# Performance work log

Measured on AMD Instinct MI355X. Metric: run time of the kernel, lower is better.

## Reference

```python
import jax, jax.numpy as jnp
import numpy as np
from jax import lax

N, T, E = 20000, 64, 640000
H, OUT, HEADS = 128, 64, 3
NEG_SLOPE = 0.2  # GATConv default negative_slope


def setup_inputs() -> dict:
    key = jax.random.key(0)
    ks = jax.random.split(key, 10)
    s = 0.1
    return {
        "node_features": jax.random.normal(ks[0], (N, T), jnp.float32),
        "edge_index": jax.random.randint(ks[1], (2, E), 0, N, dtype=jnp.int32),
        "edge_attributes": jax.random.uniform(ks[2], (E,), jnp.float32),
        "lstm_Wih": jax.random.normal(ks[3], (4 * H, 1), jnp.float32) * s,
        "lstm_Whh": jax.random.normal(ks[4], (4 * H, H), jnp.float32) * s,
        "lstm_bih": jnp.zeros((4 * H,), jnp.float32),
        "lstm_bhh": jnp.zeros((4 * H,), jnp.float32),
        "gcn_W": jax.random.normal(ks[5], (H, H), jnp.float32) * s,
        "gcn_b": jnp.zeros((H,), jnp.float32),
        "gat_W": jax.random.normal(ks[6], (HEADS * OUT, H), jnp.float32) * s,
        "gat_att_src": jax.random.normal(ks[7], (HEADS, OUT), jnp.float32) * s,
        "gat_att_dst": jax.random.normal(ks[8], (HEADS, OUT), jnp.float32) * s,
        "gat_b": jnp.zeros((HEADS * OUT,), jnp.float32),
    }


def _lstm_last(x, Wih, Whh, bih, bhh):
    """x: [N, T, 1] -> last hidden state [N, H] (torch gate order i,f,g,o)."""
    n = x.shape[0]
    h_dim = Whh.shape[1]
    b = bih + bhh

    def step(carry, xt):
        h, c = carry
        g = xt @ Wih.T + h @ Whh.T + b  # [N, 4H]
        i, f, gg, o = jnp.split(g, 4, axis=-1)
        c = jax.nn.sigmoid(f) * c + jax.nn.sigmoid(i) * jnp.tanh(gg)
        h = jax.nn.sigmoid(o) * jnp.tanh(c)
        return (h, c), None

    init = (jnp.zeros((n, h_dim), x.dtype), jnp.zeros((n, h_dim), x.dtype))
    (h, _), _ = lax.scan(step, init, jnp.swapaxes(x, 0, 1))
    return h


def _add_self_loops(row, col, n):
    loop = jnp.arange(n, dtype=row.dtype)
    return jnp.concatenate([row, loop]), jnp.concatenate([col, loop])


def _gcn(x, row, col, edge_weight, W, b):
    """PyG GCNConv: self-loops (weight 1), symmetric normalization, W x + b."""
    n = x.shape[0]
    row, col = _add_self_loops(row, col, n)
    ew = jnp.concatenate([edge_weight, jnp.ones((n,), edge_weight.dtype)])
    x = x @ W.T  # [N, H]
    deg = jax.ops.segment_sum(ew, col, num_segments=n)
    dinv = jnp.where(deg > 0, deg ** -0.5, 0.0)
    norm = dinv[row] * ew * dinv[col]  # [E+N]
    out = jax.ops.segment_sum(x[row] * norm[:, None], col, num_segments=n)
    return out + b


def _gat(x, row, col, W, att_src, att_dst, b):
    """PyG GATConv (concat=True): self-loops, edge softmax over incoming edges."""
    n = x.shape[0]
    heads, c = att_src.shape
    xh = (x @ W.T).reshape(n, heads, c)  # [N, Hd, C]
    a_src = jnp.einsum('nhc,hc->nh', xh, att_src)  # [N, Hd]
    a_dst = jnp.einsum('nhc,hc->nh', xh, att_dst)
    row, col = _add_self_loops(row, col, n)
    alpha = jax.nn.leaky_relu(a_src[row] + a_dst[col], NEG_SLOPE)  # [E', Hd]
    amax = jax.ops.segment_max(alpha, col, num_segments=n)
    alpha = jnp.exp(alpha - amax[col])
    denom = jax.ops.segment_sum(alpha, col, num_segments=n)
    alpha = alpha / denom[col]
    out = jax.ops.segment_sum(xh[row] * alpha[:, :, None], col, num_segments=n)
    return out.reshape(n, heads * c) + b


def reference(node_features, edge_index, edge_attributes,
              lstm_Wih, lstm_Whh, lstm_bih, lstm_bhh,
              gcn_W, gcn_b, gat_W, gat_att_src, gat_att_dst, gat_b):
    x = node_features[:, :, None]  # [N, T, 1]
    x = _lstm_last(x, lstm_Wih, lstm_Whh, lstm_bih, lstm_bhh)  # [N, H]
    x = jax.nn.relu(x)
    row, col = edge_index[0], edge_index[1]
    x = _gcn(x, row, col, edge_attributes, gcn_W, gcn_b)
    x = jax.nn.relu(x)
    x = _gat(x, row, col, gat_W, gat_att_src, gat_att_dst, gat_b)  # [N, Hd*C]
    return jnp.mean(x, axis=0, keepdims=True)  # global_mean_pool, batch=None -> [1, Hd*C]
```

## Files before the change

kernel.cpp:

```cpp
#include <hip/hip_runtime.h>


#define N_NODES 20000
#define T_STEPS 64
#define N_EDGES 640000
#define HDIM    128
#define JOUT    192
#define NEG_SLOPE 0.2f
#define EDGE_CAP 128
#define NBW     16
#define NGRP    6
#define NBB     (NBW * NGRP)
#define BTHR    768
#define NBLK    209
#define GRIDX   215
#define LDS_W     131072
#define LDS_BW    4096
#define LDS_SCR   (NGRP * 4096)
#define LDS_FLG   256
#define LDS_TOTAL (LDS_W + LDS_BW + LDS_SCR + LDS_FLG)

#define L2E  1.4426950408889634f
#define K2E  2.8853900817779268f

typedef _Float16 half8 __attribute__((ext_vector_type(8)));
typedef _Float16 half4v __attribute__((ext_vector_type(4)));
typedef _Float16 half2v __attribute__((ext_vector_type(2)));
typedef float floatx4 __attribute__((ext_vector_type(4)));

__device__ __forceinline__ float lrelu(float x) { return x > 0.f ? x : NEG_SLOPE * x; }

__global__ __launch_bounds__(256) void prep_kernel(
    const float* __restrict__ Whh, _Float16* __restrict__ Wpack,
    const float* __restrict__ gcnW, _Float16* __restrict__ WpackG,
    const float* __restrict__ gatW, _Float16* __restrict__ WpackA,
    int* __restrict__ cnt, float* __restrict__ deg,
    float* __restrict__ Wgt, float* __restrict__ accum)
{
  const int b = blockIdx.x;
  const int tid = threadIdx.x;
  if (b < 32) {
    int i = b * 256 + tid;
    int tile = i >> 6, lane = i & 63;
    int nt = tile >> 2, kt = tile & 3;
    int row = nt * 16 + (lane & 15);
    int c0  = kt * 32 + (lane >> 4) * 8;
    const float sc = ((row >> 7) == 2) ? K2E : L2E;
    half8 v;
    #pragma unroll
    for (int j = 0; j < 8; ++j)
      v[j] = (_Float16)(Whh[row * 128 + c0 + j] * sc);
    *(half8*)&Wpack[(size_t)i * 8] = v;
  } else if (b < 40) {
    int i = (b - 32) * 256 + tid;
    int tile = i >> 6, lane = i & 63;
    int mt = tile >> 2, kt = tile & 3;
    int row = mt * 16 + (lane & 15);
    int c0  = kt * 32 + (lane >> 4) * 8;
    half8 v;
    #pragma unroll
    for (int j = 0; j < 8; ++j) v[j] = (_Float16)gcnW[row * 128 + c0 + j];
    *(half8*)&WpackG[(size_t)i * 8] = v;
  } else if (b < 52) {
    int i = (b - 40) * 256 + tid;
    int tile = i >> 6, lane = i & 63;
    int mt = tile >> 2, kt = tile & 3;
    int row = mt * 16 + (lane & 15);
    int c0  = kt * 32 + (lane >> 4) * 8;
    half8 v;
    #pragma unroll
    for (int j = 0; j < 8; ++j) v[j] = (_Float16)gatW[row * 128 + c0 + j];
    *(half8*)&WpackA[(size_t)i * 8] = v;
  } else {
    int i = (b - 52) * 256 + tid;
    if (i < N_NODES) {
      cnt[i] = 0;
      deg[i] = 0.f;
      *(float4*)&Wgt[i * 4] = make_float4(0.f, 0.f, 0.f, 0.f);
    }
    if (i < JOUT) accum[i] = 0.f;
  }
}


#define INITACC(L, acc) do {                                                  \
  _Pragma("unroll") for (int g_ = 0; g_ < 4; ++g_) {                          \
    const float4 p0_ = *(const float4*)&bwRole[g_ * 128 + (L) * 16];          \
    const float4 p1_ = *(const float4*)&bwRole[g_ * 128 + (L) * 16 + 2];      \
    acc[g_][0] = p0_.x + xv * p0_.y;                                          \
    acc[g_][1] = p0_.z + xv * p0_.w;                                          \
    acc[g_][2] = p1_.x + xv * p1_.y;                                          \
    acc[g_][3] = p1_.z + xv * p1_.w;                                          \
  }                                                                           \
} while (0)

#define LDA(buf, L, KT) do {                                                  \
  _Pragma("unroll") for (int g_ = 0; g_ < 4; ++g_)                            \
    buf[g_] = *(const half8*)&WlRole[g_ * 16384 + (L) * 2048 + (KT) * 512];   \
} while (0)

#define MFA(acc, buf, KT) do {                                                \
  _Pragma("unroll") for (int g_ = 0; g_ < 4; ++g_)                            \
    acc[g_] = __builtin_amdgcn_mfma_f32_16x16x32_f16(                         \
        buf[g_], Bf[(KT)], acc[g_], 0, 0, 0);                                 \
} while (0)

#define PHASE4(L, acc) do {                                                   \
  const int cg_ = cgb + (L);                                                  \
  half4v hpack;                                                               \
  _Pragma("unroll") for (int r_ = 0; r_ < 4; ++r_) {                          \
    const float Be = __builtin_amdgcn_exp2f(-acc[0][r_]);                     \
    const float Ae = __builtin_amdgcn_exp2f(-acc[1][r_]);                     \
    const float De = __builtin_amdgcn_exp2f(acc[2][r_]);                      \
    const float Ee = __builtin_amdgcn_exp2f(-acc[3][r_]);                     \
    const float Ap = Ae + 1.f;                                                \
    const float Bp = Be + 1.f;                                                \
    const float Dp = De + 1.f;                                                \
    const float Nn = cst[(L) * 4 + r_] * Bp * Dp + Ap * (De - 1.f);           \
    const float cv = Nn * __builtin_amdgcn_rcpf(Ap * Bp * Dp);                \
    cst[(L) * 4 + r_] = cv;                                                   \
    const float cvc = fminf(fmaxf(cv, -10.f), 10.f);                          \
    const float Fe = __builtin_amdgcn_exp2f(K2E * cvc);                       \
    hpack[r_] = (_Float16)((Fe - 1.f) *                                       \
                __builtin_amdgcn_rcpf((Ee + 1.f) * (Fe + 1.f)));              \
  }                                                                           \
  const int lp_ = nl + 16 * (2 * (cg_ & 1) + wq_hi);                          \
  *(half4v*)&myscr[(cg_ >> 1) * 512 + lp_ * 8 + j0] = hpack;                  \
} while (0)

#define SB __builtin_amdgcn_sched_barrier(0)

#define SIGNAL(arr, val) do {                                                 \
  __threadfence_block();                                                      \
  if (ln == 0) arr[wv] = (val);                                               \
} while (0)
#define WAITGE(arr, val) do {                                                 \
  if (ln == 0) { while (arr[pw] < (val)) __builtin_amdgcn_s_sleep(1); }       \
  __builtin_amdgcn_wave_barrier();                                            \
  __threadfence_block();                                                      \
} while (0)

#define LSTM_STEP(t) do {                                                     \
  WAITGE(flW, (t));                                                           \
  half8 Bf[4];                                                                \
  _Pragma("unroll") for (int kt_ = 0; kt_ < 4; ++kt_)                         \
    Bf[kt_] = *(const half8*)&scrLane[kt_ * 512];                             \
  SIGNAL(flR, (t) + 1);                                                       \
  floatx4 accA[4], accB[4];                                                   \
  half8 Aa[4], Ab[4];                                                         \
                                                                  \
  INITACC(0, accA);                                                           \
  LDA(Aa, 0, 0); LDA(Ab, 0, 1);                                               \
  MFA(accA, Aa, 0); LDA(Aa, 0, 2);                                            \
  MFA(accA, Ab, 1); LDA(Ab, 0, 3);                                            \
  MFA(accA, Aa, 2); MFA(accA, Ab, 3);                                         \
                                                                  \
  INITACC(1, accB); LDA(Aa, 1, 0); LDA(Ab, 1, 1);                             \
  WAITGE(flR, (t) + 1);                                                       \
  SB; PHASE4(0, accA);                                                        \
  MFA(accB, Aa, 0); LDA(Aa, 1, 2);                                            \
  MFA(accB, Ab, 1); LDA(Ab, 1, 3);                                            \
  MFA(accB, Aa, 2); MFA(accB, Ab, 3);                                         \
                                                                  \
  INITACC(2, accA); LDA(Aa, 2, 0); LDA(Ab, 2, 1);                             \
  SB; PHASE4(1, accB);                                                        \
  MFA(accA, Aa, 0); LDA(Aa, 2, 2);                                            \
  MFA(accA, Ab, 1); LDA(Ab, 2, 3);                                            \
  MFA(accA, Aa, 2); MFA(accA, Ab, 3);                                         \
                                                                  \
  INITACC(3, accB); LDA(Aa, 3, 0); LDA(Ab, 3, 1);                             \
  SB; PHASE4(2, accA);                                                        \
  MFA(accB, Aa, 0); LDA(Aa, 3, 2);                                            \
  MFA(accB, Ab, 1); LDA(Ab, 3, 3);                                            \
  MFA(accB, Aa, 2); MFA(accB, Ab, 3);                                         \
  PHASE4(3, accB);                                                            \
  SIGNAL(flW, (t) + 1);                                                       \
} while (0)

__global__ __attribute__((amdgpu_flat_work_group_size(BTHR, BTHR),
                          amdgpu_waves_per_eu(3, 3)))
void lstm_stream_kernel(
    const float* __restrict__ xfeat, const _Float16* __restrict__ Wpack,
    const float* __restrict__ Wih, const float* __restrict__ bih,
    const float* __restrict__ bhh, _Float16* __restrict__ x1,
    const int* __restrict__ ei, const float* __restrict__ ew,
    int* __restrict__ cnt, int2* __restrict__ pairB, float* __restrict__ deg)
{
  extern __shared__ char dynlds[];
  const int tid  = threadIdx.x;

  if (blockIdx.x >= NBLK) {
    float* ldeg = (float*)dynlds;
    for (int i = tid; i < N_NODES; i += BTHR) ldeg[i] = 0.f;
    __syncthreads();
    const int stride = (GRIDX - NBLK) * BTHR;
    for (int e = (blockIdx.x - NBLK) * BTHR + tid; e < N_EDGES; e += stride) {
      const int r = ei[e];
      const int c = ei[N_EDGES + e];
      const float w = ew[e];
      const int p = atomicAdd(&cnt[c], 1);
      pairB[(size_t)c * EDGE_CAP + p] = make_int2(r, __float_as_int(w));
      atomicAdd(&ldeg[c], w);
    }
    __syncthreads();
    for (int i = tid; i < N_NODES; i += BTHR) {
      const float v = ldeg[i];
      if (v != 0.f) atomicAdd(&deg[i], v);
    }
    return;
  }

  _Float16* Wl  = (_Float16*)dynlds;
  float2*   bw  = (float2*)(dynlds + LDS_W);
  _Float16* scr = (_Float16*)(dynlds + LDS_W + LDS_BW);
  volatile int* flR = (volatile int*)(dynlds + LDS_W + LDS_BW + LDS_SCR);
  volatile int* flW = flR + 16;

  const int wv   = tid >> 6;
  const int pw   = wv ^ 1;
  const int grp  = wv >> 1;
  const int role = wv & 1;
  const int cgb  = role * 4;
  const int ln   = tid & 63;
  const int nl   = ln & 15;
  const int quad = ln >> 4;
  const int n0   = blockIdx.x * NBB + grp * NBW;
  const int node  = n0 + nl;
  const int nodeC = (node < N_NODES) ? node : (N_NODES - 1);

  {
    const float4* src = (const float4*)Wpack;
    float4* dst = (float4*)Wl;
    for (int i = tid; i < LDS_W / 16; i += BTHR) dst[i] = src[i];
  }
  for (int i = tid; i < 512; i += BTHR) {
    const float sc = ((i >> 7) == 2) ? K2E : L2E;
    bw[i] = make_float2((bih[i] + bhh[i]) * sc, Wih[i] * sc);
  }
  {
    float4* z = (float4*)scr;
    for (int i = tid; i < LDS_SCR / 16; i += BTHR)
      z[i] = make_float4(0.f, 0.f, 0.f, 0.f);
  }
  if (tid < 32) { flR[tid] = 0; }
  __syncthreads();

  _Float16* myscr = scr + grp * 2048;
  const _Float16* WlRole  = Wl + (size_t)cgb * 2048 + (size_t)ln * 8;
  const float2*   bwRole  = bw + cgb * 16 + quad * 4;
  const _Float16* scrLane = myscr + (size_t)ln * 8;
  const float* xrow = xfeat + (size_t)nodeC * T_STEPS;

  float cst[16];
  #pragma unroll
  for (int i = 0; i < 16; ++i) cst[i] = 0.f;

  const int wq_hi = quad >> 1;
  const int j0    = (quad & 1) * 4;

  float xv = xrow[0];

  #pragma unroll 1
  for (int t = 0; t < T_STEPS; ++t) {
    const float xn = xrow[(t + 1 <= 63) ? (t + 1) : 63];
    LSTM_STEP(t);
    xv = xn;
  }

  if (node < N_NODES) {
    #pragma unroll
    for (int k = 0; k < 2; ++k) {
      const int kt = role * 2 + k;
      half8 hf = *(const half8*)&scrLane[kt * 512];
      #pragma unroll
      for (int j = 0; j < 8; ++j)
        hf[j] = (_Float16)fmaxf((float)hf[j], 0.f);
      *(half8*)&x1[(size_t)node * HDIM + kt * 32 + quad * 8] = hf;
    }
  }
}

__global__ __launch_bounds__(256) void agg_gemm_att_kernel(
    const _Float16* __restrict__ x1, const float* __restrict__ deg,
    const int* __restrict__ cnt, const int2* __restrict__ pairB,
    const float* __restrict__ gcn_b,
    const _Float16* __restrict__ PG, const _Float16* __restrict__ PA,
    const float* __restrict__ att_src, const float* __restrict__ att_dst,
    _Float16* __restrict__ xh, float4* __restrict__ asrc,
    float4* __restrict__ adst)
{
  __shared__ float2 stg[4][64];
  __shared__ _Float16 z[16][132];
  __shared__ _Float16 zz[16][132];
  __shared__ float aS[JOUT], aD[JOUT];
  __shared__ float sAp[4][16][3], sDp[4][16][3];

  const int tid = threadIdx.x;
  const int ln = tid & 63;
  const int wv = tid >> 6;
  const int quad = ln >> 4;
  const int nl = ln & 15;
  const int nb = blockIdx.x * 16;

  for (int i = tid; i < JOUT; i += 256) { aS[i] = att_src[i]; aD[i] = att_dst[i]; }

  const half2v* x12 = (const half2v*)x1;
  #pragma unroll 1
  for (int d = 0; d < 4; ++d) {
    const int c = nb + wv * 4 + d;
    const float dc = rsqrtf(deg[c] + 1.0f);
    const half2v xc = x12[c * 64 + ln];
    float ax = (float)xc[0] * dc * dc, ay = (float)xc[1] * dc * dc;
    const int cc = cnt[c];
    const size_t base = (size_t)c * EDGE_CAP;
    for (int tb = 0; tb < cc; tb += 64) {
      const int ne = min(64, cc - tb);
      const int k = tb + ln;
      if (k < cc) {
        const int2 pr = pairB[base + k];
        stg[wv][ln] = make_float2(__int_as_float(pr.x),
            __int_as_float(pr.y) * rsqrtf(deg[pr.x] + 1.0f) * dc);
      }
      __builtin_amdgcn_wave_barrier();
      int i = 0;
      for (; i + 4 <= ne; i += 4) {
        float2 p0 = stg[wv][i],     p1 = stg[wv][i + 1];
        float2 p2 = stg[wv][i + 2], p3 = stg[wv][i + 3];
        const half2v a0 = x12[(size_t)__float_as_int(p0.x) * 64 + ln];
        const half2v a1 = x12[(size_t)__float_as_int(p1.x) * 64 + ln];
        const half2v a2 = x12[(size_t)__float_as_int(p2.x) * 64 + ln];
        const half2v a3 = x12[(size_t)__float_as_int(p3.x) * 64 + ln];
        ax += (float)a0[0] * p0.y + (float)a1[0] * p1.y +
              (float)a2[0] * p2.y + (float)a3[0] * p3.y;
        ay += (float)a0[1] * p0.y + (float)a1[1] * p1.y +
              (float)a2[1] * p2.y + (float)a3[1] * p3.y;
      }
      for (; i < ne; ++i) {
        float2 p0 = stg[wv][i];
        const half2v a0 = x12[(size_t)__float_as_int(p0.x) * 64 + ln];
        ax += (float)a0[0] * p0.y; ay += (float)a0[1] * p0.y;
      }
      __builtin_amdgcn_wave_barrier();
    }
    const int dn = wv * 4 + d;
    half2v o; o[0] = (_Float16)ax; o[1] = (_Float16)ay;
    *(half2v*)&z[dn][ln * 2] = o;
  }
  __syncthreads();

  {
    half8 Bf[4];
    #pragma unroll
    for (int kt = 0; kt < 4; ++kt)
      Bf[kt] = *(const half8*)&z[nl][kt * 32 + quad * 8];
    #pragma unroll
    for (int mm = 0; mm < 2; ++mm) {
      const int m = wv * 2 + mm;
      floatx4 acc = {0.f, 0.f, 0.f, 0.f};
      #pragma unroll
      for (int kt = 0; kt < 4; ++kt) {
        const half8 Af = *(const half8*)&PG[(size_t)((m * 4 + kt) * 64 + ln) * 8];
        acc = __builtin_amdgcn_mfma_f32_16x16x32_f16(Af, Bf[kt], acc, 0, 0, 0);
      }
      #pragma unroll
      for (int j = 0; j < 4; ++j) {
        const int jj = m * 16 + quad * 4 + j;
        zz[nl][jj] = (_Float16)fmaxf(acc[j] + gcn_b[jj], 0.f);
      }
    }
  }
  __syncthreads();

  {
    half8 Bf[4];
    #pragma unroll
    for (int kt = 0; kt < 4; ++kt)
      Bf[kt] = *(const half8*)&zz[nl][kt * 32 + quad * 8];
    float sA[3] = {0.f, 0.f, 0.f}, sD[3] = {0.f, 0.f, 0.f};
    #pragma unroll
    for (int mm = 0; mm < 3; ++mm) {
      const int m = wv * 3 + mm;
      floatx4 acc = {0.f, 0.f, 0.f, 0.f};
      #pragma unroll
      for (int kt = 0; kt < 4; ++kt) {
        const half8 Af = *(const half8*)&PA[(size_t)((m * 4 + kt) * 64 + ln) * 8];
        acc = __builtin_amdgcn_mfma_f32_16x16x32_f16(Af, Bf[kt], acc, 0, 0, 0);
      }
      const int h  = m >> 2;
      const int jo = (m & 3) * 16 + quad * 4;
      half4v o;
      #pragma unroll
      for (int j = 0; j < 4; ++j) {
        sA[h] += acc[j] * aS[h * 64 + jo + j];
        sD[h] += acc[j] * aD[h * 64 + jo + j];
        o[j] = (_Float16)acc[j];
      }
      *(half4v*)&xh[(size_t)(nb + nl) * JOUT + m * 16 + quad * 4] = o;
    }
    #pragma unroll
    for (int h = 0; h < 3; ++h) {
      sA[h] += __shfl_xor(sA[h], 16); sA[h] += __shfl_xor(sA[h], 32);
      sD[h] += __shfl_xor(sD[h], 16); sD[h] += __shfl_xor(sD[h], 32);
    }
    if (quad == 0) {
      #pragma unroll
      for (int h = 0; h < 3; ++h) {
        sAp[wv][nl][h] = sA[h];
        sDp[wv][nl][h] = sD[h];
      }
    }
  }
  __syncthreads();
  if (tid < 16) {
    float a0 = 0.f, a1 = 0.f, a2 = 0.f, d0 = 0.f, d1 = 0.f, d2 = 0.f;
    #pragma unroll
    for (int w = 0; w < 4; ++w) {
      a0 += sAp[w][tid][0]; a1 += sAp[w][tid][1]; a2 += sAp[w][tid][2];
      d0 += sDp[w][tid][0]; d1 += sDp[w][tid][1]; d2 += sDp[w][tid][2];
    }
    asrc[nb + tid] = make_float4(a0, a1, a2, 0.f);
    adst[nb + tid] = make_float4(d0, d1, d2, 0.f);
  }
}

__global__ __launch_bounds__(256) void gat_weight_kernel(
    const float4* __restrict__ asrc, const float4* __restrict__ adst,
    const int* __restrict__ cnt, const int2* __restrict__ pairB,
    float* __restrict__ W)
{
  const int lane = threadIdx.x & 63;
  const int wv = threadIdx.x >> 6;
  const int c = blockIdx.x * 4 + wv;
  const int cc = cnt[c];
  const size_t base = (size_t)c * EDGE_CAP;
  const float4 adc = adst[c];
  const float4 asc = asrc[c];
  const float se0 = __expf(lrelu(asc.x + adc.x));
  const float se1 = __expf(lrelu(asc.y + adc.y));
  const float se2 = __expf(lrelu(asc.z + adc.z));
  float dp0 = 0.f, dp1 = 0.f, dp2 = 0.f;
  float a0v[2], a1v[2], a2v[2]; int sv[2];
  #pragma unroll
  for (int it = 0; it < 2; ++it) {
    const int k = it * 64 + lane;
    sv[it] = -1;
    a0v[it] = 0.f; a1v[it] = 0.f; a2v[it] = 0.f;
    if (k < cc) {
      const int s = pairB[base + k].x;
      const float4 av = asrc[s];
      const float a0 = __expf(lrelu(av.x + adc.x));
      const float a1 = __expf(lrelu(av.y + adc.y));
      const float a2 = __expf(lrelu(av.z + adc.z));
      dp0 += a0; dp1 += a1; dp2 += a2;
      sv[it] = s; a0v[it] = a0; a1v[it] = a1; a2v[it] = a2;
    }
  }
  #pragma unroll
  for (int off = 1; off < 64; off <<= 1) {
    dp0 += __shfl_xor(dp0, off);
    dp1 += __shfl_xor(dp1, off);
    dp2 += __shfl_xor(dp2, off);
  }
  const float iv0 = 1.f / (dp0 + se0);
  const float iv1 = 1.f / (dp1 + se1);
  const float iv2 = 1.f / (dp2 + se2);
  if (lane == 0) {
    atomicAdd(&W[c * 4 + 0], se0 * iv0);
    atomicAdd(&W[c * 4 + 1], se1 * iv1);
    atomicAdd(&W[c * 4 + 2], se2 * iv2);
  }
  #pragma unroll
  for (int it = 0; it < 2; ++it) {
    if (sv[it] >= 0) {
      atomicAdd(&W[sv[it] * 4 + 0], a0v[it] * iv0);
      atomicAdd(&W[sv[it] * 4 + 1], a1v[it] * iv1);
      atomicAdd(&W[sv[it] * 4 + 2], a2v[it] * iv2);
    }
  }
}

__global__ __launch_bounds__(192) void gat_final_kernel(
    const _Float16* __restrict__ xh, const float* __restrict__ W,
    float* __restrict__ accum)
{
  const int j = threadIdx.x;
  const int h = j >> 6;
  float sum = 0.f;
  const int s0 = blockIdx.x * 80;
  for (int s = s0; s < s0 + 80; ++s)
    sum += W[s * 4 + h] * (float)xh[(size_t)s * JOUT + j];
  atomicAdd(&accum[j], sum);
}

__global__ void finalize_kernel(const float* __restrict__ accum,
                                const float* __restrict__ gat_b,
                                float* __restrict__ out)
{
  int j = threadIdx.x;
  if (j < JOUT) out[j] = accum[j] * (1.0f / N_NODES) + gat_b[j];
}

extern "C" void kernel_launch(void* const* d_in, const int* in_sizes, int n_in,
                              void* d_out, int out_size, void* d_ws, size_t ws_size,
                              hipStream_t stream)
{
  const float* xfeat = (const float*)d_in[0];
  const int*   eidx  = (const int*)d_in[1];
  const float* eattr = (const float*)d_in[2];
  const float* Wih   = (const float*)d_in[3];
  const float* Whh   = (const float*)d_in[4];
  const float* bihp  = (const float*)d_in[5];
  const float* bhhp  = (const float*)d_in[6];
  const float* gcnW  = (const float*)d_in[7];
  const float* gcnb  = (const float*)d_in[8];
  const float* gatW  = (const float*)d_in[9];
  const float* attS  = (const float*)d_in[10];
  const float* attD  = (const float*)d_in[11];
  const float* gatb  = (const float*)d_in[12];
  float* out = (float*)d_out;

  char* ws = (char*)d_ws;
  size_t off = 0;
  auto alloc = [&](size_t bytes) {
    char* p = ws + off;
    off += (bytes + 255) & ~size_t(255);
    return p;
  };
  _Float16*  x1     = (_Float16*)alloc((size_t)N_NODES * 128 * 2);
  _Float16*  xh     = (_Float16*)alloc((size_t)N_NODES * 192 * 2);
  float4*    asrc   = (float4*)alloc((size_t)N_NODES * 16);
  float4*    adst   = (float4*)alloc((size_t)N_NODES * 16);
  float*     deg    = (float*)alloc((size_t)N_NODES * 4);
  int*       cnt    = (int*)alloc((size_t)N_NODES * 4);
  int2*      pairB  = (int2*)alloc((size_t)N_NODES * EDGE_CAP * 8);
  float*     Wgt    = (float*)alloc((size_t)N_NODES * 4 * 4);
  float*     accum  = (float*)alloc(JOUT * 4);
  _Float16*  wpack  = (_Float16*)alloc(131072);
  _Float16*  wpackG = (_Float16*)alloc((size_t)128 * 128 * 2);
  _Float16*  wpackA = (_Float16*)alloc((size_t)192 * 128 * 2);

  hipFuncSetAttribute((const void*)lstm_stream_kernel,
                      hipFuncAttributeMaxDynamicSharedMemorySize, LDS_TOTAL);

  prep_kernel<<<131, 256, 0, stream>>>(Whh, wpack, gcnW, wpackG, gatW, wpackA,
                                       cnt, deg, Wgt, accum);
  lstm_stream_kernel<<<GRIDX, BTHR, LDS_TOTAL, stream>>>(
      xfeat, wpack, Wih, bihp, bhhp, x1, eidx, eattr, cnt, pairB, deg);
  agg_gemm_att_kernel<<<N_NODES / 16, 256, 0, stream>>>(
      x1, deg, cnt, pairB, gcnb, wpackG, wpackA, attS, attD, xh, asrc, adst);
  gat_weight_kernel<<<N_NODES / 4, 256, 0, stream>>>(asrc, adst, cnt, pairB, Wgt);
  gat_final_kernel<<<N_NODES / 80, 192, 0, stream>>>(xh, Wgt, accum);
  finalize_kernel<<<1, 256, 0, stream>>>(accum, gatb, out);
}
```

Baseline: 553.9 us.

## Fold weight packing into LSTM kernel and shrink prep to zeroing

Removes the separate prep kernel's Whh packing. Each LSTM block now converts Whh to scaled fp16 directly into LDS, and extra blocks in the LSTM grid pack the GCN/GAT weights and zero Wgt/accum. A small zeroing kernel handles only cnt and deg. This is meant to shorten the serial prep stage and overlap side work with the LSTM. In exchange, every LSTM block converts Whh redundantly from fp32 global memory, and the grid grows to 256 blocks with LDS-heavy filler blocks.

```diff
diff --git a/kernel.cpp b/kernel.cpp
--- a/kernel.cpp
+++ b/kernel.cpp
@@ -13,7 +13,8 @@
 #define NBB     (NBW * NGRP)
 #define BTHR    768
 #define NBLK    209
-#define GRIDX   215
+#define NEDGB   6
+#define GRIDX   256
 #define LDS_W     131072
 #define LDS_BW    4096
 #define LDS_SCR   (NGRP * 4096)
@@ -30,56 +31,11 @@
 
 __device__ __forceinline__ float lrelu(float x) { return x > 0.f ? x : NEG_SLOPE * x; }
 
-__global__ __launch_bounds__(256) void prep_kernel(
-    const float* __restrict__ Whh, _Float16* __restrict__ Wpack,
-    const float* __restrict__ gcnW, _Float16* __restrict__ WpackG,
-    const float* __restrict__ gatW, _Float16* __restrict__ WpackA,
-    int* __restrict__ cnt, float* __restrict__ deg,
-    float* __restrict__ Wgt, float* __restrict__ accum)
-{
-  const int b = blockIdx.x;
-  const int tid = threadIdx.x;
-  if (b < 32) {
-    int i = b * 256 + tid;
-    int tile = i >> 6, lane = i & 63;
-    int nt = tile >> 2, kt = tile & 3;
-    int row = nt * 16 + (lane & 15);
-    int c0  = kt * 32 + (lane >> 4) * 8;
-    const float sc = ((row >> 7) == 2) ? K2E : L2E;
-    half8 v;
-    #pragma unroll
-    for (int j = 0; j < 8; ++j)
-      v[j] = (_Float16)(Whh[row * 128 + c0 + j] * sc);
-    *(half8*)&Wpack[(size_t)i * 8] = v;
-  } else if (b < 40) {
-    int i = (b - 32) * 256 + tid;
-    int tile = i >> 6, lane = i & 63;
-    int mt = tile >> 2, kt = tile & 3;
-    int row = mt * 16 + (lane & 15);
-    int c0  = kt * 32 + (lane >> 4) * 8;
-    half8 v;
-    #pragma unroll
-    for (int j = 0; j < 8; ++j) v[j] = (_Float16)gcnW[row * 128 + c0 + j];
-    *(half8*)&WpackG[(size_t)i * 8] = v;
-  } else if (b < 52) {
-    int i = (b - 40) * 256 + tid;
-    int tile = i >> 6, lane = i & 63;
-    int mt = tile >> 2, kt = tile & 3;
-    int row = mt * 16 + (lane & 15);
-    int c0  = kt * 32 + (lane >> 4) * 8;
-    half8 v;
-    #pragma unroll
-    for (int j = 0; j < 8; ++j) v[j] = (_Float16)gatW[row * 128 + c0 + j];
-    *(half8*)&WpackA[(size_t)i * 8] = v;
-  } else {
-    int i = (b - 52) * 256 + tid;
-    if (i < N_NODES) {
-      cnt[i] = 0;
-      deg[i] = 0.f;
-      *(float4*)&Wgt[i * 4] = make_float4(0.f, 0.f, 0.f, 0.f);
-    }
-    if (i < JOUT) accum[i] = 0.f;
-  }
+__global__ __launch_bounds__(256) void zero0_kernel(
+    int* __restrict__ cnt, float* __restrict__ deg)
+{
+  int i = blockIdx.x * 256 + threadIdx.x;
+  if (i < N_NODES) { cnt[i] = 0; deg[i] = 0.f; }
 }
 
 
@@ -180,20 +136,58 @@
 __global__ __attribute__((amdgpu_flat_work_group_size(BTHR, BTHR),
                           amdgpu_waves_per_eu(3, 3)))
 void lstm_stream_kernel(
-    const float* __restrict__ xfeat, const _Float16* __restrict__ Wpack,
+    const float* __restrict__ xfeat, const float* __restrict__ Whh,
     const float* __restrict__ Wih, const float* __restrict__ bih,
     const float* __restrict__ bhh, _Float16* __restrict__ x1,
     const int* __restrict__ ei, const float* __restrict__ ew,
-    int* __restrict__ cnt, int2* __restrict__ pairB, float* __restrict__ deg)
+    int* __restrict__ cnt, int2* __restrict__ pairB, float* __restrict__ deg,
+    const float* __restrict__ gcnW, _Float16* __restrict__ WpackG,
+    const float* __restrict__ gatW, _Float16* __restrict__ WpackA,
+    float* __restrict__ Wgt, float* __restrict__ accum)
 {
   extern __shared__ char dynlds[];
   const int tid  = threadIdx.x;
+
+  if (blockIdx.x >= NBLK + NEDGB) {
+    const int ab = blockIdx.x - (NBLK + NEDGB);
+    if (ab < 3) {
+      int i = ab * BTHR + tid;
+      if (i < 2048) {
+        int tile = i >> 6, lane = i & 63;
+        int mt = tile >> 2, kt = tile & 3;
+        int row = mt * 16 + (lane & 15);
+        int c0  = kt * 32 + (lane >> 4) * 8;
+        half8 v;
+        #pragma unroll
+        for (int j = 0; j < 8; ++j) v[j] = (_Float16)gcnW[row * 128 + c0 + j];
+        *(half8*)&WpackG[(size_t)i * 8] = v;
+      }
+    } else if (ab < 7) {
+      int i = (ab - 3) * BTHR + tid;
+      if (i < 3072) {
+        int tile = i >> 6, lane = i & 63;
+        int mt = tile >> 2, kt = tile & 3;
+        int row = mt * 16 + (lane & 15);
+        int c0  = kt * 32 + (lane >> 4) * 8;
+        half8 v;
+        #pragma unroll
+        for (int j = 0; j < 8; ++j) v[j] = (_Float16)gatW[row * 128 + c0 + j];
+        *(half8*)&WpackA[(size_t)i * 8] = v;
+      }
+    } else {
+      const int a0 = (ab - 7) * BTHR + tid;
+      for (int i = a0; i < N_NODES; i += 34 * BTHR)
+        *(float4*)&Wgt[i * 4] = make_float4(0.f, 0.f, 0.f, 0.f);
+      if (ab == 7 && tid < JOUT) accum[tid] = 0.f;
+    }
+    return;
+  }
 
   if (blockIdx.x >= NBLK) {
     float* ldeg = (float*)dynlds;
     for (int i = tid; i < N_NODES; i += BTHR) ldeg[i] = 0.f;
     __syncthreads();
-    const int stride = (GRIDX - NBLK) * BTHR;
+    const int stride = NEDGB * BTHR;
     for (int e = (blockIdx.x - NBLK) * BTHR + tid; e < N_EDGES; e += stride) {
       const int r = ei[e];
       const int c = ei[N_EDGES + e];
@@ -228,10 +222,20 @@
   const int node  = n0 + nl;
   const int nodeC = (node < N_NODES) ? node : (N_NODES - 1);
 
-  {
-    const float4* src = (const float4*)Wpack;
-    float4* dst = (float4*)Wl;
-    for (int i = tid; i < LDS_W / 16; i += BTHR) dst[i] = src[i];
+  for (int i = tid; i < 8192; i += BTHR) {
+    const int tile = i >> 6, lane = i & 63;
+    const int nt = tile >> 2, kt = tile & 3;
+    const int row = nt * 16 + (lane & 15);
+    const int c0  = kt * 32 + (lane >> 4) * 8;
+    const float sc = ((row >> 7) == 2) ? K2E : L2E;
+    const float4 w0 = *(const float4*)&Whh[row * 128 + c0];
+    const float4 w1 = *(const float4*)&Whh[row * 128 + c0 + 4];
+    half8 v;
+    v[0] = (_Float16)(w0.x * sc); v[1] = (_Float16)(w0.y * sc);
+    v[2] = (_Float16)(w0.z * sc); v[3] = (_Float16)(w0.w * sc);
+    v[4] = (_Float16)(w1.x * sc); v[5] = (_Float16)(w1.y * sc);
+    v[6] = (_Float16)(w1.z * sc); v[7] = (_Float16)(w1.w * sc);
+    *(half8*)&Wl[(size_t)i * 8] = v;
   }
   for (int i = tid; i < 512; i += BTHR) {
     const float sc = ((i >> 7) == 2) ? K2E : L2E;
@@ -535,17 +539,16 @@
   int2*      pairB  = (int2*)alloc((size_t)N_NODES * EDGE_CAP * 8);
   float*     Wgt    = (float*)alloc((size_t)N_NODES * 4 * 4);
   float*     accum  = (float*)alloc(JOUT * 4);
-  _Float16*  wpack  = (_Float16*)alloc(131072);
   _Float16*  wpackG = (_Float16*)alloc((size_t)128 * 128 * 2);
   _Float16*  wpackA = (_Float16*)alloc((size_t)192 * 128 * 2);
 
   hipFuncSetAttribute((const void*)lstm_stream_kernel,
                       hipFuncAttributeMaxDynamicSharedMemorySize, LDS_TOTAL);
 
-  prep_kernel<<<131, 256, 0, stream>>>(Whh, wpack, gcnW, wpackG, gatW, wpackA,
-                                       cnt, deg, Wgt, accum);
+  zero0_kernel<<<(N_NODES + 255) / 256, 256, 0, stream>>>(cnt, deg);
   lstm_stream_kernel<<<GRIDX, BTHR, LDS_TOTAL, stream>>>(
-      xfeat, wpack, Wih, bihp, bhhp, x1, eidx, eattr, cnt, pairB, deg);
+      xfeat, Whh, Wih, bihp, bhhp, x1, eidx, eattr, cnt, pairB, deg,
+      gcnW, wpackG, gatW, wpackA, Wgt, accum);
   agg_gemm_att_kernel<<<N_NODES / 16, 256, 0, stream>>>(
       x1, deg, cnt, pairB, gcnb, wpackG, wpackA, attS, attD, xh, asrc, adst);
   gat_weight_kernel<<<N_NODES / 4, 256, 0, stream>>>(asrc, adst, cnt, pairB, Wgt);
```

Result: no change. 557.0 us (+0.6%).
